# Kernel optimization log

Measured on AMD Instinct MI355X. Metric: run time of the kernel, lower is better.

## Reference

```python
import jax, jax.numpy as jnp
import numpy as np

LN_EPS = 1e-5
N_NODES = 50000
IN_DIM = 128
OUT_DIM = 128
N_EDGES = 800000


def _ln(x, g, b):
    m = jnp.mean(x, axis=-1, keepdims=True)
    v = jnp.mean((x - m) ** 2, axis=-1, keepdims=True)
    return (x - m) * jax.lax.rsqrt(v + LN_EPS) * g + b


def setup_inputs() -> dict:
    key = jax.random.key(0)
    ks = jax.random.split(key, 16)

    def lin(k, fan_in, fan_out):
        return jax.random.normal(k, (fan_in, fan_out), dtype=jnp.float32) / np.sqrt(fan_in)

    x = jax.random.normal(ks[0], (N_NODES, IN_DIM), dtype=jnp.float32)
    edge_index = jax.random.randint(ks[1], (2, N_EDGES), 0, N_NODES, dtype=jnp.int64)
    return {
        "x": x,
        "edge_index": edge_index,
        # transform: Linear(in,out) + LayerNorm
        "W1": lin(ks[2], IN_DIM, OUT_DIM), "b1": jnp.zeros((OUT_DIM,), jnp.float32),
        "g1": jnp.ones((OUT_DIM,), jnp.float32), "bt1": jnp.zeros((OUT_DIM,), jnp.float32),
        # edge_attention: Linear(2*out,out) -> ReLU -> Linear(out,1) -> Sigmoid
        "We1": lin(ks[3], 2 * OUT_DIM, OUT_DIM), "be1": jnp.zeros((OUT_DIM,), jnp.float32),
        "We2": lin(ks[4], OUT_DIM, 1), "be2": jnp.zeros((1,), jnp.float32),
        # node_attention: Linear(out,out) -> ReLU -> Linear(out,1) -> Sigmoid (computed, unused)
        "Wn1": lin(ks[5], OUT_DIM, OUT_DIM), "bn1": jnp.zeros((OUT_DIM,), jnp.float32),
        "Wn2": lin(ks[6], OUT_DIM, 1), "bn2": jnp.zeros((1,), jnp.float32),
        # update_gate: Linear(2*out,out) -> Sigmoid
        "Wg": lin(ks[7], 2 * OUT_DIM, OUT_DIM), "bg": jnp.zeros((OUT_DIM,), jnp.float32),
        # final LayerNorm
        "g2": jnp.ones((OUT_DIM,), jnp.float32), "bt2": jnp.zeros((OUT_DIM,), jnp.float32),
    }


def reference(x, edge_index, W1, b1, g1, bt1, We1, be1, We2, be2,
              Wn1, bn1, Wn2, bn2, Wg, bg, g2, bt2):
    n = x.shape[0]
    # transform: Linear -> LayerNorm -> ReLU (Dropout is identity in eval)
    h = jax.nn.relu(_ln(x @ W1 + b1, g1, bt1))           # [N, D]
    row, col = edge_index[0], edge_index[1]
    h_src = h[row]                                        # [E, D]
    ef = jnp.concatenate([h_src, h[col]], axis=1)         # [E, 2D]
    edge_weights = jax.nn.sigmoid(jax.nn.relu(ef @ We1 + be1) @ We2 + be2)[:, 0]  # [E]
    # node_weights computed in original forward but never used in the output
    node_weights = jax.nn.sigmoid(jax.nn.relu(h @ Wn1 + bn1) @ Wn2 + bn2)[:, 0]
    _ = node_weights
    # weighted scatter-add: aggr[dst] += edge_weights[i] * h[src]
    aggr = jax.ops.segment_sum(edge_weights[:, None] * h_src, col, num_segments=n)  # [N, D]
    gate = jax.nn.sigmoid(jnp.concatenate([h, aggr], axis=-1) @ Wg + bg)
    h_new = gate * aggr + (1.0 - gate) * h
    return _ln(h_new, g2, bt2)
```

## Files before the change

### kernel.cpp

```cpp
#include <hip/hip_runtime.h>
#include <math.h>

#define D 128
#define NT 32
#define LP 132
#define SCB 64
#define HB 256

__device__ __forceinline__ float wave_allsum(float v) {
    #pragma unroll
    for (int off = 32; off; off >>= 1) v += __shfl_xor(v, off);
    return v;
}

__global__ void __launch_bounds__(256) fused_hist_transform(
    const int* __restrict__ ei, int* __restrict__ deg, int E,
    const float* __restrict__ x, const float* __restrict__ W1, const float* __restrict__ b1,
    const float* __restrict__ g1, const float* __restrict__ bt1,
    const float* __restrict__ We1, const float* __restrict__ be1,
    float* __restrict__ AH, float* __restrict__ B, int N)
{
    if (blockIdx.x < HB) {
        for (int e = blockIdx.x * 256 + threadIdx.x; e < E; e += HB * 256)
            atomicAdd(&deg[ei[E + e]], 1);
        return;
    }
    __shared__ float xs[NT][LP];
    const int t = threadIdx.x;
    const int q = t >> 6, lane = t & 63;
    const int c = lane;
    const int base = (blockIdx.x - HB) * NT;

    {
        int node = t >> 3, c0 = (t & 7) * 16;
        int gn = min(base + node, N - 1);
        const float4* src = (const float4*)(x + (size_t)gn * D + c0);
        float4* dst = (float4*)&xs[node][c0];
        dst[0] = src[0]; dst[1] = src[1]; dst[2] = src[2]; dst[3] = src[3];
    }

    float acc[8][2];
    #pragma unroll
    for (int n = 0; n < 8; ++n) { acc[n][0] = 0.f; acc[n][1] = 0.f; }
    for (int k = 0; k < 128; k += 4) {
        float w00 = W1[(k+0)*128 + c], w01 = W1[(k+0)*128 + c + 64];
        float w10 = W1[(k+1)*128 + c], w11 = W1[(k+1)*128 + c + 64];
        float w20 = W1[(k+2)*128 + c], w21 = W1[(k+2)*128 + c + 64];
        float w30 = W1[(k+3)*128 + c], w31 = W1[(k+3)*128 + c + 64];
        #pragma unroll
        for (int n = 0; n < 8; ++n) {
            float4 xv = *(const float4*)&xs[q*8+n][k];
            acc[n][0] += xv.x*w00 + xv.y*w10 + xv.z*w20 + xv.w*w30;
            acc[n][1] += xv.x*w01 + xv.y*w11 + xv.z*w21 + xv.w*w31;
        }
    }

    {
        float b0 = b1[c], b1v = b1[c + 64];
        float gg0 = g1[c], gg1 = g1[c + 64];
        float bb0 = bt1[c], bb1 = bt1[c + 64];
        #pragma unroll
        for (int n = 0; n < 8; ++n) {
            int node = q * 8 + n;
            float v0 = acc[n][0] + b0, v1 = acc[n][1] + b1v;
            float s = wave_allsum(v0 + v1);
            float qq = wave_allsum(v0*v0 + v1*v1);
            float m = s * (1.f/128.f);
            float var = qq * (1.f/128.f) - m*m;
            float rs = rsqrtf(var + 1e-5f);
            float h0 = fmaxf((v0 - m)*rs*gg0 + bb0, 0.f);
            float h1 = fmaxf((v1 - m)*rs*gg1 + bb1, 0.f);
            xs[node][c]      = h0;
            xs[node][c + 64] = h1;
            int gn = base + node;
            if (gn < N) {
                AH[(size_t)gn * 256 + 128 + c]      = h0;
                AH[(size_t)gn * 256 + 128 + c + 64] = h1;
            }
        }
    }

    float aA[8][2], aB[8][2];
    #pragma unroll
    for (int n = 0; n < 8; ++n) { aA[n][0]=0.f; aA[n][1]=0.f; aB[n][0]=0.f; aB[n][1]=0.f; }
    for (int k = 0; k < 128; k += 4) {
        float t00 = We1[(k+0)*128 + c],   t01 = We1[(k+0)*128 + c + 64];
        float t10 = We1[(k+1)*128 + c],   t11 = We1[(k+1)*128 + c + 64];
        float t20 = We1[(k+2)*128 + c],   t21 = We1[(k+2)*128 + c + 64];
        float t30 = We1[(k+3)*128 + c],   t31 = We1[(k+3)*128 + c + 64];
        float u00 = We1[(k+128)*128 + c], u01 = We1[(k+128)*128 + c + 64];
        float u10 = We1[(k+129)*128 + c], u11 = We1[(k+129)*128 + c + 64];
        float u20 = We1[(k+130)*128 + c], u21 = We1[(k+130)*128 + c + 64];
        float u30 = We1[(k+131)*128 + c], u31 = We1[(k+131)*128 + c + 64];
        #pragma unroll
        for (int n = 0; n < 8; ++n) {
            float4 hv = *(const float4*)&xs[q*8+n][k];
            aA[n][0] += hv.x*t00 + hv.y*t10 + hv.z*t20 + hv.w*t30;
            aA[n][1] += hv.x*t01 + hv.y*t11 + hv.z*t21 + hv.w*t31;
            aB[n][0] += hv.x*u00 + hv.y*u10 + hv.z*u20 + hv.w*u30;
            aB[n][1] += hv.x*u01 + hv.y*u11 + hv.z*u21 + hv.w*u31;
        }
    }
    {
        float be0 = be1[c], be1v = be1[c + 64];
        #pragma unroll
        for (int n = 0; n < 8; ++n) {
            int gn = base + q*8 + n;
            if (gn < N) {
                AH[(size_t)gn * 256 + c]      = aA[n][0] + be0;
                AH[(size_t)gn * 256 + c + 64] = aA[n][1] + be1v;
                B[(size_t)gn * D + c]         = aB[n][0];
                B[(size_t)gn * D + c + 64]    = aB[n][1];
            }
        }
    }
}

__global__ void __launch_bounds__(256) scan_a(const int* __restrict__ deg,
                                              int* __restrict__ bsum, int N) {
    __shared__ int red[256];
    const int b = blockIdx.x, t = threadIdx.x;
    const int C = (N + SCB - 1) / SCB;
    const int W = (C + 255) / 256;
    int s0 = b * C + t * W;
    int s1 = min(s0 + W, min((b + 1) * C, N));
    int s = 0;
    for (int i = s0; i < s1; ++i) s += deg[i];
    red[t] = s;
    __syncthreads();
    #pragma unroll
    for (int d = 128; d; d >>= 1) {
        if (t < d) red[t] += red[t + d];
        __syncthreads();
    }
    if (t == 0) bsum[b] = red[0];
}

__global__ void __launch_bounds__(256) scan_c(const int* __restrict__ deg,
                                              const int* __restrict__ bsum,
                                              int* __restrict__ off,
                                              int* __restrict__ cursor, int N) {
    __shared__ int pre[256];
    __shared__ int bofs;
    const int b = blockIdx.x, t = threadIdx.x;
    const int C = (N + SCB - 1) / SCB;
    const int W = (C + 255) / 256;
    if (t == 0) {
        int r = 0;
        for (int i = 0; i < b; ++i) r += bsum[i];
        bofs = r;
        if (b == SCB - 1) off[N] = r + bsum[b];
    }
    int s0 = b * C + t * W;
    int s1 = min(s0 + W, min((b + 1) * C, N));
    int s = 0;
    for (int i = s0; i < s1; ++i) s += deg[i];
    pre[t] = s;
    __syncthreads();
    for (int d = 1; d < 256; d <<= 1) {
        int vv = (t >= d) ? pre[t - d] : 0;
        __syncthreads();
        if (t >= d) pre[t] += vv;
        __syncthreads();
    }
    int run = bofs + ((t == 0) ? 0 : pre[t - 1]);
    for (int i = s0; i < s1; ++i) {
        off[i] = run;
        cursor[i] = run;
        run += deg[i];
    }
}

__global__ void __launch_bounds__(256) scatter_kernel(const int* __restrict__ ei,
                                                      int* __restrict__ cursor,
                                                      int* __restrict__ ssrc, int E) {
    int e = blockIdx.x * 256 + threadIdx.x;
    if (e < E) {
        int pos = atomicAdd(&cursor[ei[E + e]], 1);
        ssrc[pos] = ei[e];
    }
}

__global__ void __launch_bounds__(256) agg_v7(
    const int* __restrict__ off, const int* __restrict__ ssrc,
    const float* __restrict__ AH, const float* __restrict__ B,
    const float* __restrict__ We2, const float* __restrict__ be2,
    float* __restrict__ aggr, int N)
{
    const int wid = threadIdx.x >> 6, lane = threadIdx.x & 63;
    const int node = blockIdx.x * 4 + wid;
    if (node >= N) return;
    const int g = lane >> 4;
    const int c8 = (lane & 15) * 8;

    const int s = off[node], e = off[node + 1];
    const int deg = e - s;

    if (deg <= 0) {
        if (g == 0) {
            float4 z = make_float4(0.f,0.f,0.f,0.f);
            float4* Op = (float4*)(aggr + (size_t)node * D + c8);
            Op[0] = z; Op[1] = z;
        }
        return;
    }

    const float4* Bp = (const float4*)(B + (size_t)node * D + c8);
    float4 b0 = Bp[0], b1 = Bp[1];
    const float4* Wp = (const float4*)(We2 + c8);
    float4 w0 = Wp[0], w1 = Wp[1];
    const float be = be2[0];

    float4 acc0 = make_float4(0.f,0.f,0.f,0.f);
    float4 acc1 = make_float4(0.f,0.f,0.f,0.f);

    if (deg <= 64) {
        int myidx = ssrc[min(s + lane, e - 1)];
        const int nit = (deg + 7) >> 3;
        for (int it = 0; it < nit; ++it) {
            int ja = it * 8 + g * 2;
            int jb = ja + 1;
            int sa = __shfl(myidx, min(ja, deg - 1));
            int sb = __shfl(myidx, min(jb, deg - 1));
            const float4* Ra = (const float4*)(AH + (size_t)sa * 256 + c8);
            const float4* Rb = (const float4*)(AH + (size_t)sb * 256 + c8);
            float4 aa0 = Ra[0], aa1 = Ra[1];
            float4 ha0 = Ra[32], ha1 = Ra[33];
            float4 ab0 = Rb[0], ab1 = Rb[1];
            float4 hb0 = Rb[32], hb1 = Rb[33];
            float da = fmaxf(aa0.x + b0.x, 0.f) * w0.x + fmaxf(aa0.y + b0.y, 0.f) * w0.y
                     + fmaxf(aa0.z + b0.z, 0.f) * w0.z + fmaxf(aa0.w + b0.w, 0.f) * w0.w
                     + fmaxf(aa1.x + b1.x, 0.f) * w1.x + fmaxf(aa1.y + b1.y, 0.f) * w1.y
                     + fmaxf(aa1.z + b1.z, 0.f) * w1.z + fmaxf(aa1.w + b1.w, 0.f) * w1.w;
            float db = fmaxf(ab0.x + b0.x, 0.f) * w0.x + fmaxf(ab0.y + b0.y, 0.f) * w0.y
                     + fmaxf(ab0.z + b0.z, 0.f) * w0.z + fmaxf(ab0.w + b0.w, 0.f) * w0.w
                     + fmaxf(ab1.x + b1.x, 0.f) * w1.x + fmaxf(ab1.y + b1.y, 0.f) * w1.y
                     + fmaxf(ab1.z + b1.z, 0.f) * w1.z + fmaxf(ab1.w + b1.w, 0.f) * w1.w;
            da += __shfl_xor(da, 1);  db += __shfl_xor(db, 1);
            da += __shfl_xor(da, 2);  db += __shfl_xor(db, 2);
            da += __shfl_xor(da, 4);  db += __shfl_xor(db, 4);
            da += __shfl_xor(da, 8);  db += __shfl_xor(db, 8);
            float wa = (ja < deg) ? 1.f / (1.f + expf(-(da + be))) : 0.f;
            float wb = (jb < deg) ? 1.f / (1.f + expf(-(db + be))) : 0.f;
            acc0.x += wa * ha0.x + wb * hb0.x; acc0.y += wa * ha0.y + wb * hb0.y;
            acc0.z += wa * ha0.z + wb * hb0.z; acc0.w += wa * ha0.w + wb * hb0.w;
            acc1.x += wa * ha1.x + wb * hb1.x; acc1.y += wa * ha1.y + wb * hb1.y;
            acc1.z += wa * ha1.z + wb * hb1.z; acc1.w += wa * ha1.w + wb * hb1.w;
        }
    } else {
        const int nit = (deg + 7) >> 3;
        for (int it = 0; it < nit; ++it) {
            int ja = s + it * 8 + g * 2;
            int jb = ja + 1;
            int sa = ssrc[min(ja, e - 1)];
            int sb = ssrc[min(jb, e - 1)];
            const float4* Ra = (const float4*)(AH + (size_t)sa * 256 + c8);
            const float4* Rb = (const float4*)(AH + (size_t)sb * 256 + c8);
            float4 aa0 = Ra[0], aa1 = Ra[1];
            float4 ha0 = Ra[32], ha1 = Ra[33];
            float4 ab0 = Rb[0], ab1 = Rb[1];
            float4 hb0 = Rb[32], hb1 = Rb[33];
            float da = fmaxf(aa0.x + b0.x, 0.f) * w0.x + fmaxf(aa0.y + b0.y, 0.f) * w0.y
                     + fmaxf(aa0.z + b0.z, 0.f) * w0.z + fmaxf(aa0.w + b0.w, 0.f) * w0.w
                     + fmaxf(aa1.x + b1.x, 0.f) * w1.x + fmaxf(aa1.y + b1.y, 0.f) * w1.y
                     + fmaxf(aa1.z + b1.z, 0.f) * w1.z + fmaxf(aa1.w + b1.w, 0.f) * w1.w;
            float db = fmaxf(ab0.x + b0.x, 0.f) * w0.x + fmaxf(ab0.y + b0.y, 0.f) * w0.y
                     + fmaxf(ab0.z + b0.z, 0.f) * w0.z + fmaxf(ab0.w + b0.w, 0.f) * w0.w
                     + fmaxf(ab1.x + b1.x, 0.f) * w1.x + fmaxf(ab1.y + b1.y, 0.f) * w1.y
                     + fmaxf(ab1.z + b1.z, 0.f) * w1.z + fmaxf(ab1.w + b1.w, 0.f) * w1.w;
            da += __shfl_xor(da, 1);  db += __shfl_xor(db, 1);
            da += __shfl_xor(da, 2);  db += __shfl_xor(db, 2);
            da += __shfl_xor(da, 4);  db += __shfl_xor(db, 4);
            da += __shfl_xor(da, 8);  db += __shfl_xor(db, 8);
            float wa = (ja < e) ? 1.f / (1.f + expf(-(da + be))) : 0.f;
            float wb = (jb < e) ? 1.f / (1.f + expf(-(db + be))) : 0.f;
            acc0.x += wa * ha0.x + wb * hb0.x; acc0.y += wa * ha0.y + wb * hb0.y;
            acc0.z += wa * ha0.z + wb * hb0.z; acc0.w += wa * ha0.w + wb * hb0.w;
            acc1.x += wa * ha1.x + wb * hb1.x; acc1.y += wa * ha1.y + wb * hb1.y;
            acc1.z += wa * ha1.z + wb * hb1.z; acc1.w += wa * ha1.w + wb * hb1.w;
        }
    }

    #pragma unroll
    for (int o = 16; o <= 32; o <<= 1) {
        acc0.x += __shfl_xor(acc0.x, o); acc0.y += __shfl_xor(acc0.y, o);
        acc0.z += __shfl_xor(acc0.z, o); acc0.w += __shfl_xor(acc0.w, o);
        acc1.x += __shfl_xor(acc1.x, o); acc1.y += __shfl_xor(acc1.y, o);
        acc1.z += __shfl_xor(acc1.z, o); acc1.w += __shfl_xor(acc1.w, o);
    }
    if (g == 0) {
        float4* Op = (float4*)(aggr + (size_t)node * D + c8);
        Op[0] = acc0;
        Op[1] = acc1;
    }
}

__global__ void __launch_bounds__(256) gate_v6(
    const float* __restrict__ AH, const float* __restrict__ aggr,
    const float* __restrict__ Wg, const float* __restrict__ bg,
    const float* __restrict__ g2, const float* __restrict__ bt2,
    float* __restrict__ out, int N)
{
    __shared__ float ts[NT][LP];
    const int t = threadIdx.x;
    const int q = t >> 6, lane = t & 63;
    const int c = lane;
    const int base = blockIdx.x * NT;

    {
        int node = t >> 3, c0 = (t & 7) * 16;
        size_t g = (size_t)min(base + node, N - 1) * 256 + 128 + c0;
        const float4* src = (const float4*)(AH + g);
        float4* dst = (float4*)&ts[node][c0];
        dst[0] = src[0]; dst[1] = src[1]; dst[2] = src[2]; dst[3] = src[3];
    }

    float hv[8][2];
    #pragma unroll
    for (int n = 0; n < 8; ++n) {
        hv[n][0] = ts[q*8+n][c];
        hv[n][1] = ts[q*8+n][c + 64];
    }

    float acc[8][2];
    #pragma unroll
    for (int n = 0; n < 8; ++n) { acc[n][0] = 0.f; acc[n][1] = 0.f; }
    for (int k = 0; k < 128; k += 4) {
        float t00 = Wg[(k+0)*128 + c], t01 = Wg[(k+0)*128 + c + 64];
        float t10 = Wg[(k+1)*128 + c], t11 = Wg[(k+1)*128 + c + 64];
        float t20 = Wg[(k+2)*128 + c], t21 = Wg[(k+2)*128 + c + 64];
        float t30 = Wg[(k+3)*128 + c], t31 = Wg[(k+3)*128 + c + 64];
        #pragma unroll
        for (int n = 0; n < 8; ++n) {
            float4 v = *(const float4*)&ts[q*8+n][k];
            acc[n][0] += v.x*t00 + v.y*t10 + v.z*t20 + v.w*t30;
            acc[n][1] += v.x*t01 + v.y*t11 + v.z*t21 + v.w*t31;
        }
    }

    {
        int node = t >> 3, c0 = (t & 7) * 16;
        size_t g = (size_t)min(base + node, N - 1) * D + c0;
        const float4* src = (const float4*)(aggr + g);
        float4* dst = (float4*)&ts[node][c0];
        dst[0] = src[0]; dst[1] = src[1]; dst[2] = src[2]; dst[3] = src[3];
    }

    for (int k = 0; k < 128; k += 4) {
        float u00 = Wg[(k+128)*128 + c], u01 = Wg[(k+128)*128 + c + 64];
        float u10 = Wg[(k+129)*128 + c], u11 = Wg[(k+129)*128 + c + 64];
        float u20 = Wg[(k+130)*128 + c], u21 = Wg[(k+130)*128 + c + 64];
        float u30 = Wg[(k+131)*128 + c], u31 = Wg[(k+131)*128 + c + 64];
        #pragma unroll
        for (int n = 0; n < 8; ++n) {
            float4 v = *(const float4*)&ts[q*8+n][k];
            acc[n][0] += v.x*u00 + v.y*u10 + v.z*u20 + v.w*u30;
            acc[n][1] += v.x*u01 + v.y*u11 + v.z*u21 + v.w*u31;
        }
    }

    {
        float bg0 = bg[c], bg1 = bg[c + 64];
        float gg0 = g2[c], gg1 = g2[c + 64];
        float bb0 = bt2[c], bb1 = bt2[c + 64];
        #pragma unroll
        for (int n = 0; n < 8; ++n) {
            int node = q*8 + n;
            float av0 = ts[node][c], av1 = ts[node][c + 64];
            float ga = 1.f / (1.f + expf(-(acc[n][0] + bg0)));
            float gb = 1.f / (1.f + expf(-(acc[n][1] + bg1)));
            float y0 = ga * av0 + (1.f - ga) * hv[n][0];
            float y1 = gb * av1 + (1.f - gb) * hv[n][1];
            float s = wave_allsum(y0 + y1);
            float qq = wave_allsum(y0*y0 + y1*y1);
            float m = s * (1.f/128.f);
            float var = qq * (1.f/128.f) - m*m;
            float rs = rsqrtf(var + 1e-5f);
            int gn = base + node;
            if (gn < N) {
                out[(size_t)gn * D + c]      = (y0 - m)*rs*gg0 + bb0;
                out[(size_t)gn * D + c + 64] = (y1 - m)*rs*gg1 + bb1;
            }
        }
    }
}

extern "C" void kernel_launch(void* const* d_in, const int* in_sizes, int n_in,
                              void* d_out, int out_size, void* d_ws, size_t ws_size,
                              hipStream_t stream) {
    const float* x   = (const float*)d_in[0];
    const int*   ei  = (const int*)d_in[1];
    const float* W1  = (const float*)d_in[2];
    const float* b1  = (const float*)d_in[3];
    const float* g1  = (const float*)d_in[4];
    const float* bt1 = (const float*)d_in[5];
    const float* We1 = (const float*)d_in[6];
    const float* be1 = (const float*)d_in[7];
    const float* We2 = (const float*)d_in[8];
    const float* be2 = (const float*)d_in[9];
    const float* Wg  = (const float*)d_in[14];
    const float* bg  = (const float*)d_in[15];
    const float* g2  = (const float*)d_in[16];
    const float* bt2 = (const float*)d_in[17];

    const int N = in_sizes[0] / D;
    const int E = in_sizes[1] / 2;
    const size_t ND = (size_t)N * D;

    float* AH   = (float*)d_ws;
    float* B    = AH + 2 * ND;
    float* aggr = B + ND;
    int* deg    = (int*)(aggr + ND);
    int* off    = deg + (N + 1);
    int* cursor = off + (N + 1);
    int* ssrc   = cursor + (N + 1);
    int* bsum   = ssrc + E;

    (void)hipMemsetAsync(deg, 0, (size_t)(N + 1) * sizeof(int), stream);

    const int nblkT = (N + NT - 1) / NT;
    fused_hist_transform<<<HB + nblkT, 256, 0, stream>>>(
        ei, deg, E, x, W1, b1, g1, bt1, We1, be1, AH, B, N);
    scan_a<<<SCB, 256, 0, stream>>>(deg, bsum, N);
    scan_c<<<SCB, 256, 0, stream>>>(deg, bsum, off, cursor, N);
    scatter_kernel<<<(E + 255) / 256, 256, 0, stream>>>(ei, cursor, ssrc, E);
    agg_v7<<<(N + 3) / 4, 256, 0, stream>>>(off, ssrc, AH, B, We2, be2, aggr, N);
    gate_v6<<<nblkT, 256, 0, stream>>>(AH, aggr, Wg, bg, g2, bt2, (float*)d_out, N);
}
```

Baseline: 380.1 us.

## Split K across half-waves with float4 weight loads in transform and gate GEMMs

```diff
diff --git a/kernel.cpp b/kernel.cpp
--- a/kernel.cpp
+++ b/kernel.cpp
@@ -28,7 +28,9 @@
     __shared__ float xs[NT][LP];
     const int t = threadIdx.x;
     const int q = t >> 6, lane = t & 63;
-    const int c = lane;
+    const int cg = (lane & 31) * 4;
+    const int kh = (lane >> 5) * 64;
+    const int khi = lane >> 5;
     const int base = (blockIdx.x - HB) * NT;
 
     {
@@ -39,78 +41,103 @@
         dst[0] = src[0]; dst[1] = src[1]; dst[2] = src[2]; dst[3] = src[3];
     }
 
-    float acc[8][2];
-    #pragma unroll
-    for (int n = 0; n < 8; ++n) { acc[n][0] = 0.f; acc[n][1] = 0.f; }
-    for (int k = 0; k < 128; k += 4) {
-        float w00 = W1[(k+0)*128 + c], w01 = W1[(k+0)*128 + c + 64];
-        float w10 = W1[(k+1)*128 + c], w11 = W1[(k+1)*128 + c + 64];
-        float w20 = W1[(k+2)*128 + c], w21 = W1[(k+2)*128 + c + 64];
-        float w30 = W1[(k+3)*128 + c], w31 = W1[(k+3)*128 + c + 64];
+    float4 acc[8];
+    #pragma unroll
+    for (int n = 0; n < 8; ++n) acc[n] = make_float4(0.f,0.f,0.f,0.f);
+    for (int k4 = 0; k4 < 16; ++k4) {
+        int k = kh + k4 * 4;
+        float4 w0 = *(const float4*)&W1[(k+0) * 128 + cg];
+        float4 w1 = *(const float4*)&W1[(k+1) * 128 + cg];
+        float4 w2 = *(const float4*)&W1[(k+2) * 128 + cg];
+        float4 w3 = *(const float4*)&W1[(k+3) * 128 + cg];
         #pragma unroll
         for (int n = 0; n < 8; ++n) {
             float4 xv = *(const float4*)&xs[q*8+n][k];
-            acc[n][0] += xv.x*w00 + xv.y*w10 + xv.z*w20 + xv.w*w30;
-            acc[n][1] += xv.x*w01 + xv.y*w11 + xv.z*w21 + xv.w*w31;
-        }
-    }
-
-    {
-        float b0 = b1[c], b1v = b1[c + 64];
-        float gg0 = g1[c], gg1 = g1[c + 64];
-        float bb0 = bt1[c], bb1 = bt1[c + 64];
+            acc[n].x += xv.x*w0.x + xv.y*w1.x + xv.z*w2.x + xv.w*w3.x;
+            acc[n].y += xv.x*w0.y + xv.y*w1.y + xv.z*w2.y + xv.w*w3.y;
+            acc[n].z += xv.x*w0.z + xv.y*w1.z + xv.z*w2.z + xv.w*w3.z;
+            acc[n].w += xv.x*w0.w + xv.y*w1.w + xv.z*w2.w + xv.w*w3.w;
+        }
+    }
+    #pragma unroll
+    for (int n = 0; n < 8; ++n) {
+        acc[n].x += __shfl_xor(acc[n].x, 32);
+        acc[n].y += __shfl_xor(acc[n].y, 32);
+        acc[n].z += __shfl_xor(acc[n].z, 32);
+        acc[n].w += __shfl_xor(acc[n].w, 32);
+    }
+
+    {
+        float4 b4 = *(const float4*)&b1[cg];
+        float4 g4 = *(const float4*)&g1[cg];
+        float4 t4 = *(const float4*)&bt1[cg];
         #pragma unroll
         for (int n = 0; n < 8; ++n) {
             int node = q * 8 + n;
-            float v0 = acc[n][0] + b0, v1 = acc[n][1] + b1v;
-            float s = wave_allsum(v0 + v1);
-            float qq = wave_allsum(v0*v0 + v1*v1);
+            float v0 = acc[n].x + b4.x, v1 = acc[n].y + b4.y;
+            float v2 = acc[n].z + b4.z, v3 = acc[n].w + b4.w;
+            float s  = wave_allsum(v0 + v1 + v2 + v3) * 0.5f;
+            float qq = wave_allsum(v0*v0 + v1*v1 + v2*v2 + v3*v3) * 0.5f;
             float m = s * (1.f/128.f);
             float var = qq * (1.f/128.f) - m*m;
             float rs = rsqrtf(var + 1e-5f);
-            float h0 = fmaxf((v0 - m)*rs*gg0 + bb0, 0.f);
-            float h1 = fmaxf((v1 - m)*rs*gg1 + bb1, 0.f);
-            xs[node][c]      = h0;
-            xs[node][c + 64] = h1;
-            int gn = base + node;
-            if (gn < N) {
-                AH[(size_t)gn * 256 + 128 + c]      = h0;
-                AH[(size_t)gn * 256 + 128 + c + 64] = h1;
+            float4 h4;
+            h4.x = fmaxf((v0 - m)*rs*g4.x + t4.x, 0.f);
+            h4.y = fmaxf((v1 - m)*rs*g4.y + t4.y, 0.f);
+            h4.z = fmaxf((v2 - m)*rs*g4.z + t4.z, 0.f);
+            h4.w = fmaxf((v3 - m)*rs*g4.w + t4.w, 0.f);
+            if (khi == 0) {
+                *(float4*)&xs[node][cg] = h4;
+                int gn = base + node;
+                if (gn < N) *(float4*)&AH[(size_t)gn * 256 + 128 + cg] = h4;
             }
         }
     }
 
-    float aA[8][2], aB[8][2];
-    #pragma unroll
-    for (int n = 0; n < 8; ++n) { aA[n][0]=0.f; aA[n][1]=0.f; aB[n][0]=0.f; aB[n][1]=0.f; }
-    for (int k = 0; k < 128; k += 4) {
-        float t00 = We1[(k+0)*128 + c],   t01 = We1[(k+0)*128 + c + 64];
-        float t10 = We1[(k+1)*128 + c],   t11 = We1[(k+1)*128 + c + 64];
-        float t20 = We1[(k+2)*128 + c],   t21 = We1[(k+2)*128 + c + 64];
-        float t30 = We1[(k+3)*128 + c],   t31 = We1[(k+3)*128 + c + 64];
-        float u00 = We1[(k+128)*128 + c], u01 = We1[(k+128)*128 + c + 64];
-        float u10 = We1[(k+129)*128 + c], u11 = We1[(k+129)*128 + c + 64];
-        float u20 = We1[(k+130)*128 + c], u21 = We1[(k+130)*128 + c + 64];
-        float u30 = We1[(k+131)*128 + c], u31 = We1[(k+131)*128 + c + 64];
+    float4 aA[8], aB[8];
+    #pragma unroll
+    for (int n = 0; n < 8; ++n) { aA[n] = make_float4(0.f,0.f,0.f,0.f); aB[n] = make_float4(0.f,0.f,0.f,0.f); }
+    for (int k4 = 0; k4 < 16; ++k4) {
+        int k = kh + k4 * 4;
+        float4 t0 = *(const float4*)&We1[(k+0) * 128 + cg];
+        float4 t1 = *(const float4*)&We1[(k+1) * 128 + cg];
+        float4 t2 = *(const float4*)&We1[(k+2) * 128 + cg];
+        float4 t3 = *(const float4*)&We1[(k+3) * 128 + cg];
+        float4 u0 = *(const float4*)&We1[(k+128) * 128 + cg];
+        float4 u1 = *(const float4*)&We1[(k+129) * 128 + cg];
+        float4 u2 = *(const float4*)&We1[(k+130) * 128 + cg];
+        float4 u3 = *(const float4*)&We1[(k+131) * 128 + cg];
         #pragma unroll
         for (int n = 0; n < 8; ++n) {
             float4 hv = *(const float4*)&xs[q*8+n][k];
-            aA[n][0] += hv.x*t00 + hv.y*t10 + hv.z*t20 + hv.w*t30;
-            aA[n][1] += hv.x*t01 + hv.y*t11 + hv.z*t21 + hv.w*t31;
-            aB[n][0] += hv.x*u00 + hv.y*u10 + hv.z*u20 + hv.w*u30;
-            aB[n][1] += hv.x*u01 + hv.y*u11 + hv.z*u21 + hv.w*u31;
-        }
-    }
-    {
-        float be0 = be1[c], be1v = be1[c + 64];
-        #pragma unroll
-        for (int n = 0; n < 8; ++n) {
+            aA[n].x += hv.x*t0.x + hv.y*t1.x + hv.z*t2.x + hv.w*t3.x;
+            aA[n].y += hv.x*t0.y + hv.y*t1.y + hv.z*t2.y + hv.w*t3.y;
+            aA[n].z += hv.x*t0.z + hv.y*t1.z + hv.z*t2.z + hv.w*t3.z;
+            aA[n].w += hv.x*t0.w + hv.y*t1.w + hv.z*t2.w + hv.w*t3.w;
+            aB[n].x += hv.x*u0.x + hv.y*u1.x + hv.z*u2.x + hv.w*u3.x;
+            aB[n].y += hv.x*u0.y + hv.y*u1.y + hv.z*u2.y + hv.w*u3.y;
+            aB[n].z += hv.x*u0.z + hv.y*u1.z + hv.z*u2.z + hv.w*u3.z;
+            aB[n].w += hv.x*u0.w + hv.y*u1.w + hv.z*u2.w + hv.w*u3.w;
+        }
+    }
+    {
+        float4 be4 = *(const float4*)&be1[cg];
+        #pragma unroll
+        for (int n = 0; n < 8; ++n) {
+            aA[n].x += __shfl_xor(aA[n].x, 32);
+            aA[n].y += __shfl_xor(aA[n].y, 32);
+            aA[n].z += __shfl_xor(aA[n].z, 32);
+            aA[n].w += __shfl_xor(aA[n].w, 32);
+            aB[n].x += __shfl_xor(aB[n].x, 32);
+            aB[n].y += __shfl_xor(aB[n].y, 32);
+            aB[n].z += __shfl_xor(aB[n].z, 32);
+            aB[n].w += __shfl_xor(aB[n].w, 32);
             int gn = base + q*8 + n;
-            if (gn < N) {
-                AH[(size_t)gn * 256 + c]      = aA[n][0] + be0;
-                AH[(size_t)gn * 256 + c + 64] = aA[n][1] + be1v;
-                B[(size_t)gn * D + c]         = aB[n][0];
-                B[(size_t)gn * D + c + 64]    = aB[n][1];
+            if (khi == 0 && gn < N) {
+                float4 a4 = make_float4(aA[n].x + be4.x, aA[n].y + be4.y,
+                                        aA[n].z + be4.z, aA[n].w + be4.w);
+                *(float4*)&AH[(size_t)gn * 256 + cg] = a4;
+                *(float4*)&B[(size_t)gn * D + cg]    = aB[n];
             }
         }
     }
@@ -295,7 +322,7 @@
     }
 }
 
-__global__ void __launch_bounds__(256) gate_v6(
+__global__ void __launch_bounds__(256) gate_v10(
     const float* __restrict__ AH, const float* __restrict__ aggr,
     const float* __restrict__ Wg, const float* __restrict__ bg,
     const float* __restrict__ g2, const float* __restrict__ bt2,
@@ -304,7 +331,9 @@
     __shared__ float ts[NT][LP];
     const int t = threadIdx.x;
     const int q = t >> 6, lane = t & 63;
-    const int c = lane;
+    const int cg = (lane & 31) * 4;
+    const int kh = (lane >> 5) * 64;
+    const int khi = lane >> 5;
     const int base = blockIdx.x * NT;
 
     {
@@ -315,26 +344,26 @@
         dst[0] = src[0]; dst[1] = src[1]; dst[2] = src[2]; dst[3] = src[3];
     }
 
-    float hv[8][2];
-    #pragma unroll
-    for (int n = 0; n < 8; ++n) {
-        hv[n][0] = ts[q*8+n][c];
-        hv[n][1] = ts[q*8+n][c + 64];
-    }
-
-    float acc[8][2];
-    #pragma unroll
-    for (int n = 0; n < 8; ++n) { acc[n][0] = 0.f; acc[n][1] = 0.f; }
-    for (int k = 0; k < 128; k += 4) {
-        float t00 = Wg[(k+0)*128 + c], t01 = Wg[(k+0)*128 + c + 64];
-        float t10 = Wg[(k+1)*128 + c], t11 = Wg[(k+1)*128 + c + 64];
-        float t20 = Wg[(k+2)*128 + c], t21 = Wg[(k+2)*128 + c + 64];
-        float t30 = Wg[(k+3)*128 + c], t31 = Wg[(k+3)*128 + c + 64];
+    float4 hv[8];
+    #pragma unroll
+    for (int n = 0; n < 8; ++n) hv[n] = *(const float4*)&ts[q*8+n][cg];
+
+    float4 acc[8];
+    #pragma unroll
+    for (int n = 0; n < 8; ++n) acc[n] = make_float4(0.f,0.f,0.f,0.f);
+    for (int k4 = 0; k4 < 16; ++k4) {
+        int k = kh + k4 * 4;
+        float4 w0 = *(const float4*)&Wg[(k+0) * 128 + cg];
+        float4 w1 = *(const float4*)&Wg[(k+1) * 128 + cg];
+        float4 w2 = *(const float4*)&Wg[(k+2) * 128 + cg];
+        float4 w3 = *(const float4*)&Wg[(k+3) * 128 + cg];
         #pragma unroll
         for (int n = 0; n < 8; ++n) {
             float4 v = *(const float4*)&ts[q*8+n][k];
-            acc[n][0] += v.x*t00 + v.y*t10 + v.z*t20 + v.w*t30;
-            acc[n][1] += v.x*t01 + v.y*t11 + v.z*t21 + v.w*t31;
+            acc[n].x += v.x*w0.x + v.y*w1.x + v.z*w2.x + v.w*w3.x;
+            acc[n].y += v.x*w0.y + v.y*w1.y + v.z*w2.y + v.w*w3.y;
+            acc[n].z += v.x*w0.z + v.y*w1.z + v.z*w2.z + v.w*w3.z;
+            acc[n].w += v.x*w0.w + v.y*w1.w + v.z*w2.w + v.w*w3.w;
         }
     }
 
@@ -346,40 +375,58 @@
         dst[0] = src[0]; dst[1] = src[1]; dst[2] = src[2]; dst[3] = src[3];
     }
 
-    for (int k = 0; k < 128; k += 4) {
-        float u00 = Wg[(k+128)*128 + c], u01 = Wg[(k+128)*128 + c + 64];
-        float u10 = Wg[(k+129)*128 + c], u11 = Wg[(k+129)*128 + c + 64];
-        float u20 = Wg[(k+130)*128 + c], u21 = Wg[(k+130)*128 + c + 64];
-        float u30 = Wg[(k+131)*128 + c], u31 = Wg[(k+131)*128 + c + 64];
+    for (int k4 = 0; k4 < 16; ++k4) {
+        int k = kh + k4 * 4;
+        float4 w0 = *(const float4*)&Wg[(k+128) * 128 + cg];
+        float4 w1 = *(const float4*)&Wg[(k+129) * 128 + cg];
+        float4 w2 = *(const float4*)&Wg[(k+130) * 128 + cg];
+        float4 w3 = *(const float4*)&Wg[(k+131) * 128 + cg];
         #pragma unroll
         for (int n = 0; n < 8; ++n) {
             float4 v = *(const float4*)&ts[q*8+n][k];
-            acc[n][0] += v.x*u00 + v.y*u10 + v.z*u20 + v.w*u30;
-            acc[n][1] += v.x*u01 + v.y*u11 + v.z*u21 + v.w*u31;
-        }
-    }
-
-    {
-        float bg0 = bg[c], bg1 = bg[c + 64];
-        float gg0 = g2[c], gg1 = g2[c + 64];
-        float bb0 = bt2[c], bb1 = bt2[c + 64];
+            acc[n].x += v.x*w0.x + v.y*w1.x + v.z*w2.x + v.w*w3.x;
+            acc[n].y += v.x*w0.y + v.y*w1.y + v.z*w2.y + v.w*w3.y;
+            acc[n].z += v.x*w0.z + v.y*w1.z + v.z*w2.z + v.w*w3.z;
+            acc[n].w += v.x*w0.w + v.y*w1.w + v.z*w2.w + v.w*w3.w;
+        }
+    }
+    #pragma unroll
+    for (int n = 0; n < 8; ++n) {
+        acc[n].x += __shfl_xor(acc[n].x, 32);
+        acc[n].y += __shfl_xor(acc[n].y, 32);
+        acc[n].z += __shfl_xor(acc[n].z, 32);
+        acc[n].w += __shfl_xor(acc[n].w, 32);
+    }
+
+    {
+        float4 bg4 = *(const float4*)&bg[cg];
+        float4 gg4 = *(const float4*)&g2[cg];
+        float4 bb4 = *(const float4*)&bt2[cg];
         #pragma unroll
         for (int n = 0; n < 8; ++n) {
             int node = q*8 + n;
-            float av0 = ts[node][c], av1 = ts[node][c + 64];
-            float ga = 1.f / (1.f + expf(-(acc[n][0] + bg0)));
-            float gb = 1.f / (1.f + expf(-(acc[n][1] + bg1)));
-            float y0 = ga * av0 + (1.f - ga) * hv[n][0];
-            float y1 = gb * av1 + (1.f - gb) * hv[n][1];
-            float s = wave_allsum(y0 + y1);
-            float qq = wave_allsum(y0*y0 + y1*y1);
+            float4 av = *(const float4*)&ts[node][cg];
+            float g0 = 1.f / (1.f + expf(-(acc[n].x + bg4.x)));
+            float g1v = 1.f / (1.f + expf(-(acc[n].y + bg4.y)));
+            float g2v = 1.f / (1.f + expf(-(acc[n].z + bg4.z)));
+            float g3 = 1.f / (1.f + expf(-(acc[n].w + bg4.w)));
+            float y0 = g0 * av.x + (1.f - g0) * hv[n].x;
+            float y1 = g1v * av.y + (1.f - g1v) * hv[n].y;
+            float y2 = g2v * av.z + (1.f - g2v) * hv[n].z;
+            float y3 = g3 * av.w + (1.f - g3) * hv[n].w;
+            float s  = wave_allsum(y0 + y1 + y2 + y3) * 0.5f;
+            float qq = wave_allsum(y0*y0 + y1*y1 + y2*y2 + y3*y3) * 0.5f;
             float m = s * (1.f/128.f);
             float var = qq * (1.f/128.f) - m*m;
             float rs = rsqrtf(var + 1e-5f);
             int gn = base + node;
-            if (gn < N) {
-                out[(size_t)gn * D + c]      = (y0 - m)*rs*gg0 + bb0;
-                out[(size_t)gn * D + c + 64] = (y1 - m)*rs*gg1 + bb1;
+            if (khi == 0 && gn < N) {
+                float4 o4;
+                o4.x = (y0 - m)*rs*gg4.x + bb4.x;
+                o4.y = (y1 - m)*rs*gg4.y + bb4.y;
+                o4.z = (y2 - m)*rs*gg4.z + bb4.z;
+                o4.w = (y3 - m)*rs*gg4.w + bb4.w;
+                *(float4*)&out[(size_t)gn * D + cg] = o4;
             }
         }
     }
@@ -425,5 +472,5 @@
     scan_c<<<SCB, 256, 0, stream>>>(deg, bsum, off, cursor, N);
     scatter_kernel<<<(E + 255) / 256, 256, 0, stream>>>(ei, cursor, ssrc, E);
     agg_v7<<<(N + 3) / 4, 256, 0, stream>>>(off, ssrc, AH, B, We2, be2, aggr, N);
-    gate_v6<<<nblkT, 256, 0, stream>>>(AH, aggr, Wg, bg, g2, bt2, (float*)d_out, N);
-}
+    gate_v10<<<nblkT, 256, 0, stream>>>(AH, aggr, Wg, bg, g2, bt2, (float*)d_out, N);
+}
```

After: 375.5 us. About the same (-1.2%).
